# Kernel tuning notes

Measured on AMD Instinct MI355X. Metric: run time of the kernel, lower is better.

## Reference

```python
import jax, jax.numpy as jnp
import numpy as np

B, N, D, H = 4, 512, 3, 128


def _linear_params(key, fan_in, fan_out):
    kw, kb = jax.random.split(key)
    lim = 1.0 / np.sqrt(fan_in)
    W = jax.random.uniform(kw, (fan_in, fan_out), jnp.float32, -lim, lim)
    b = jax.random.uniform(kb, (fan_out,), jnp.float32, -lim, lim)
    return W, b


def setup_inputs() -> dict:
    key = jax.random.key(0)
    ks = jax.random.split(key, 9)
    x = jax.random.normal(ks[0], (B, N, D), jnp.float32)
    Ws1, bs1 = _linear_params(ks[1], D, H)   # make_features.single
    Wp1, bp1 = _linear_params(ks[2], D, H)   # make_features.pair
    Wc1s, bc1s = _linear_params(ks[3], H, H)  # combine1.single
    Wc1p, bc1p = _linear_params(ks[4], H, H)  # combine1.pair
    Wpl, bpl = _linear_params(ks[5], H, H)    # pair_lin
    Wc2s, bc2s = _linear_params(ks[6], H, D)  # combine2.single (random, not zero-init, to exercise full graph)
    Wc2p, bc2p = _linear_params(ks[7], H, D)  # combine2.pair
    Wskip = -jnp.eye(D, dtype=jnp.float32)    # skip.weight init = -I (applied as x @ Wskip.T)
    return dict(x=x, Ws1=Ws1, bs1=bs1, Wp1=Wp1, bp1=bp1,
                Wc1s=Wc1s, bc1s=bc1s, Wc1p=Wc1p, bc1p=bc1p,
                Wpl=Wpl, bpl=bpl, Wc2s=Wc2s, bc2s=bc2s,
                Wc2p=Wc2p, bc2p=bc2p, Wskip=Wskip)


def reference(x, Ws1, bs1, Wp1, bp1, Wc1s, bc1s, Wc1p, bc1p,
              Wpl, bpl, Wc2s, bc2s, Wc2p, bc2p, Wskip):
    ht = lambda v: jnp.clip(v, -1.0, 1.0)  # Hardtanh
    n = x.shape[-2]
    # pairs[..., i, j, :] = x[j] - x[i]
    pairs = x[..., None, :, :] - x[..., :, None, :]          # [B, N, N, D]
    s = ht(x @ Ws1 + bs1)                                    # [B, N, H]
    p = ht(pairs @ Wp1 + bp1)                                # [B, N, N, H]
    # combine1: single(s) + pair(p).sum(dim=-3); sum-then-matmul is identical math, cheaper
    s = s @ Wc1s + bc1s + (p.sum(axis=-3) @ Wc1p + n * bc1p)  # [B, N, H]
    p = p @ Wpl + bpl                                         # [B, N, N, H]
    s = ht(s)
    p = ht(p)
    out = s @ Wc2s + bc2s + (p.sum(axis=-3) @ Wc2p + n * bc2p)  # [B, N, D]
    out = out + x @ Wskip.T                                     # skip (bias-free linear)
    return out
```

## Files before the change

### kernel.cpp

```cpp
#include <hip/hip_runtime.h>
#include <hip/hip_bf16.h>


typedef float f32x4 __attribute__((ext_vector_type(4)));
typedef __bf16 bf16x8 __attribute__((ext_vector_type(8)));

union PKU { uint4 u; bf16x8 v; };

__device__ __forceinline__ float clamp1(float v) { return fminf(1.0f, fmaxf(-1.0f, v)); }
__device__ __forceinline__ unsigned f2bf(float f) {
    unsigned u = __float_as_uint(f);
    u += 0x7FFF + ((u >> 16) & 1);
    return u >> 16;
}

__global__ void prep_kernel(const float* __restrict__ x, const float* __restrict__ Wp1,
                            const float* __restrict__ Wpl,
                            float* __restrict__ q, unsigned* __restrict__ wsBf) {
    int gid = blockIdx.x * 256 + threadIdx.x;
    if (blockIdx.x < 1024) {
        int h = gid & 127, n = gid >> 7;
        const float* xp = x + n * 3;
        q[gid] = xp[0] * Wp1[h] + xp[1] * Wp1[128 + h] + xp[2] * Wp1[256 + h];
    } else {
        int g = gid - 1024 * 256;
        int w  = g & 3;
        int l  = (g >> 2) & 63;
        int fi = g >> 8;
        int wn = fi >> 4, nf = (fi >> 2) & 3, kf = fi & 3;
        int n = wn * 64 + nf * 16 + (l & 15);
        int k = kf * 32 + (l >> 4) * 8 + w * 2;
        unsigned lo = f2bf(Wpl[k * 128 + n]);
        unsigned hi = f2bf(Wpl[(k + 1) * 128 + n]);
        wsBf[g] = lo | (hi << 16);
    }
}

__global__ __launch_bounds__(256, 2) void pair_kernel(
    const float* __restrict__ q, const unsigned* __restrict__ wsBf,
    const float* __restrict__ bp1, const float* __restrict__ bpl,
    float* __restrict__ psum1, float* __restrict__ psum2)
{
    __shared__ uint4 A_lds[2048];
    __shared__ float ps1[16][128];
    __shared__ float ps2[2][128];

    const int tid  = threadIdx.x;
    const int lane = tid & 63;
    const int wid  = tid >> 6;
    const int wm = wid >> 1, wn = wid & 1;
    const int bj = blockIdx.x;
    const int b  = bj >> 9;
    const float* __restrict__ qb = q + (b << 9) * 128;

    bf16x8 Bf[4][4];
    #pragma unroll
    for (int nf = 0; nf < 4; ++nf)
        #pragma unroll
        for (int kf = 0; kf < 4; ++kf) {
            PKU t;
            t.u = *(const uint4*)(wsBf + ((((wn << 4) | (nf << 2) | kf) << 6) | lane) * 4);
            Bf[nf][kf] = t.v;
        }

    const int c = tid & 15, rb = tid >> 4;
    float qjb[8];
    {
        const float* qj = q + bj * 128 + c * 8;
        #pragma unroll
        for (int e = 0; e < 8; ++e) qjb[e] = qj[e] + bp1[c * 8 + e];
    }
    float bplv[4];
    #pragma unroll
    for (int nf = 0; nf < 4; ++nf) bplv[nf] = bpl[wn * 64 + nf * 16 + (lane & 15)];

    float psum1r[8] = {0, 0, 0, 0, 0, 0, 0, 0};
    f32x4 acc[4][4];
    #pragma unroll
    for (int mf = 0; mf < 4; ++mf)
        #pragma unroll
        for (int nf = 0; nf < 4; ++nf) acc[mf][nf] = (f32x4){0.f, 0.f, 0.f, 0.f};
    float colsum[4] = {0, 0, 0, 0};

    for (int ch = 0; ch < 4; ++ch) {
        #pragma unroll
        for (int u = 0; u < 8; ++u) {
            const int r = (u << 4) | rb;
            const int i = (ch << 7) | r;
            const float4 q0 = *(const float4*)(qb + i * 128 + c * 8);
            const float4 q1 = *(const float4*)(qb + i * 128 + c * 8 + 4);
            float p[8];
            p[0] = clamp1(qjb[0] - q0.x); p[1] = clamp1(qjb[1] - q0.y);
            p[2] = clamp1(qjb[2] - q0.z); p[3] = clamp1(qjb[3] - q0.w);
            p[4] = clamp1(qjb[4] - q1.x); p[5] = clamp1(qjb[5] - q1.y);
            p[6] = clamp1(qjb[6] - q1.z); p[7] = clamp1(qjb[7] - q1.w);
            #pragma unroll
            for (int e = 0; e < 8; ++e) psum1r[e] += p[e];
            uint4 pk;
            pk.x = f2bf(p[0]) | (f2bf(p[1]) << 16);
            pk.y = f2bf(p[2]) | (f2bf(p[3]) << 16);
            pk.z = f2bf(p[4]) | (f2bf(p[5]) << 16);
            pk.w = f2bf(p[6]) | (f2bf(p[7]) << 16);
            unsigned addr = (r << 8) | (c << 4);
            addr ^= ((r & 7) << 4);
            A_lds[addr >> 4] = pk;
        }
        __syncthreads();
        #pragma unroll
        for (int kf = 0; kf < 4; ++kf) {
            bf16x8 Af[4];
            #pragma unroll
            for (int mf = 0; mf < 4; ++mf) {
                const int row = wm * 64 + mf * 16 + (lane & 15);
                unsigned addr = (row << 8) + (kf << 6) + ((lane >> 4) << 4);
                addr ^= ((row & 7) << 4);
                PKU t; t.u = A_lds[addr >> 4];
                Af[mf] = t.v;
            }
            #pragma unroll
            for (int mf = 0; mf < 4; ++mf)
                #pragma unroll
                for (int nf = 0; nf < 4; ++nf)
                    acc[mf][nf] = __builtin_amdgcn_mfma_f32_16x16x32_bf16(
                        Af[mf], Bf[nf][kf], acc[mf][nf], 0, 0, 0);
        }
        __syncthreads();
        #pragma unroll
        for (int mf = 0; mf < 4; ++mf)
            #pragma unroll
            for (int nf = 0; nf < 4; ++nf) {
                f32x4 a = acc[mf][nf];
                acc[mf][nf] = (f32x4){0.f, 0.f, 0.f, 0.f};
                colsum[nf] += clamp1(a.x + bplv[nf]) + clamp1(a.y + bplv[nf])
                            + clamp1(a.z + bplv[nf]) + clamp1(a.w + bplv[nf]);
            }
    }

    *(float4*)(&ps1[rb][c * 8])     = make_float4(psum1r[0], psum1r[1], psum1r[2], psum1r[3]);
    *(float4*)(&ps1[rb][c * 8 + 4]) = make_float4(psum1r[4], psum1r[5], psum1r[6], psum1r[7]);
    #pragma unroll
    for (int nf = 0; nf < 4; ++nf) {
        float v = colsum[nf];
        v += __shfl_xor(v, 16);
        v += __shfl_xor(v, 32);
        if (lane < 16) ps2[wm][wn * 64 + nf * 16 + lane] = v;
    }
    __syncthreads();
    if (tid < 128) {
        float s = 0.f;
        #pragma unroll
        for (int r2 = 0; r2 < 16; ++r2) s += ps1[r2][tid];
        psum1[bj * 128 + tid] = s;
        psum2[bj * 128 + tid] = ps2[0][tid] + ps2[1][tid];
    }
}

__global__ void combine_kernel(
    const float* __restrict__ x,
    const float* __restrict__ Ws1, const float* __restrict__ bs1,
    const float* __restrict__ Wc1s, const float* __restrict__ bc1s,
    const float* __restrict__ Wc1p, const float* __restrict__ bc1p,
    const float* __restrict__ Wc2s, const float* __restrict__ bc2s,
    const float* __restrict__ Wc2p, const float* __restrict__ bc2p,
    const float* __restrict__ Wskip,
    const float* __restrict__ psum1, const float* __restrict__ psum2,
    float* __restrict__ out)
{
    __shared__ float s1[128], p1s[128], red[6];
    const int h = threadIdx.x;
    const int bj = blockIdx.x;
    const float* xj = x + bj * 3;

    float s1h = clamp1(xj[0] * Ws1[h] + xj[1] * Ws1[128 + h] + xj[2] * Ws1[256 + h] + bs1[h]);
    s1[h]  = s1h;
    p1s[h] = psum1[bj * 128 + h];
    __syncthreads();

    float s2 = bc1s[h] + 512.0f * bc1p[h];
    for (int k = 0; k < 128; ++k)
        s2 += s1[k] * Wc1s[k * 128 + h] + p1s[k] * Wc1p[k * 128 + h];
    float s3 = clamp1(s2);

    float ps2h = psum2[bj * 128 + h];
    float c0 = s3 * Wc2s[h * 3 + 0] + ps2h * Wc2p[h * 3 + 0];
    float c1 = s3 * Wc2s[h * 3 + 1] + ps2h * Wc2p[h * 3 + 1];
    float c2 = s3 * Wc2s[h * 3 + 2] + ps2h * Wc2p[h * 3 + 2];
    #pragma unroll
    for (int off = 32; off > 0; off >>= 1) {
        c0 += __shfl_down(c0, off);
        c1 += __shfl_down(c1, off);
        c2 += __shfl_down(c2, off);
    }
    if ((h & 63) == 0) {
        red[(h >> 6) * 3 + 0] = c0;
        red[(h >> 6) * 3 + 1] = c1;
        red[(h >> 6) * 3 + 2] = c2;
    }
    __syncthreads();
    if (h < 3) {
        float o = red[h] + red[3 + h];
        o += bc2s[h] + 512.0f * bc2p[h];
        o += xj[0] * Wskip[h * 3 + 0] + xj[1] * Wskip[h * 3 + 1] + xj[2] * Wskip[h * 3 + 2];
        out[bj * 3 + h] = o;
    }
}

extern "C" void kernel_launch(void* const* d_in, const int* in_sizes, int n_in,
                              void* d_out, int out_size, void* d_ws, size_t ws_size,
                              hipStream_t stream) {
    const float* x    = (const float*)d_in[0];
    const float* Ws1  = (const float*)d_in[1];
    const float* bs1  = (const float*)d_in[2];
    const float* Wp1  = (const float*)d_in[3];
    const float* bp1  = (const float*)d_in[4];
    const float* Wc1s = (const float*)d_in[5];
    const float* bc1s = (const float*)d_in[6];
    const float* Wc1p = (const float*)d_in[7];
    const float* bc1p = (const float*)d_in[8];
    const float* Wpl  = (const float*)d_in[9];
    const float* bpl  = (const float*)d_in[10];
    const float* Wc2s = (const float*)d_in[11];
    const float* bc2s = (const float*)d_in[12];
    const float* Wc2p = (const float*)d_in[13];
    const float* bc2p = (const float*)d_in[14];
    const float* Wskip= (const float*)d_in[15];

    float*    q    = (float*)d_ws;
    unsigned* wsBf = (unsigned*)((char*)d_ws + (1 << 20));
    float*    ps1  = (float*)((char*)d_ws + (1 << 20) + 32768);
    float*    ps2  = ps1 + 4 * 512 * 128;

    prep_kernel<<<1056, 256, 0, stream>>>(x, Wp1, Wpl, q, wsBf);
    pair_kernel<<<2048, 256, 0, stream>>>(q, wsBf, bp1, bpl, ps1, ps2);
    combine_kernel<<<2048, 128, 0, stream>>>(x, Ws1, bs1, Wc1s, bc1s, Wc1p, bc1p,
                                             Wc2s, bc2s, Wc2p, bc2p, Wskip,
                                             ps1, ps2, (float*)d_out);
}
```

Baseline: 167.0 us.

## Fuse combine stage into pair kernel and double-buffer the LDS A tile

```diff
diff --git a/kernel.cpp b/kernel.cpp
--- a/kernel.cpp
+++ b/kernel.cpp
@@ -7,22 +7,29 @@
 
 union PKU { uint4 u; bf16x8 v; };
 
-__device__ __forceinline__ float clamp1(float v) { return fminf(1.0f, fmaxf(-1.0f, v)); }
+__device__ __forceinline__ float ht1(float v) { return __builtin_amdgcn_fmed3f(v, -1.0f, 1.0f); }
 __device__ __forceinline__ unsigned f2bf(float f) {
     unsigned u = __float_as_uint(f);
     u += 0x7FFF + ((u >> 16) & 1);
     return u >> 16;
 }
+__device__ __forceinline__ unsigned cvtpk(float a, float b) {
+    unsigned r;
+    asm("v_cvt_pk_bf16_f32 %0, %1, %2" : "=v"(r) : "v"(a), "v"(b));
+    return r;
+}
 
 __global__ void prep_kernel(const float* __restrict__ x, const float* __restrict__ Wp1,
                             const float* __restrict__ Wpl,
-                            float* __restrict__ q, unsigned* __restrict__ wsBf) {
+                            const float* __restrict__ Wc1s, const float* __restrict__ Wc1p,
+                            float* __restrict__ q, unsigned* __restrict__ wsBf,
+                            float* __restrict__ wt1s, float* __restrict__ wt1p) {
     int gid = blockIdx.x * 256 + threadIdx.x;
     if (blockIdx.x < 1024) {
         int h = gid & 127, n = gid >> 7;
         const float* xp = x + n * 3;
         q[gid] = xp[0] * Wp1[h] + xp[1] * Wp1[128 + h] + xp[2] * Wp1[256 + h];
-    } else {
+    } else if (blockIdx.x < 1056) {
         int g = gid - 1024 * 256;
         int w  = g & 3;
         int l  = (g >> 2) & 63;
@@ -33,17 +40,32 @@
         unsigned lo = f2bf(Wpl[k * 128 + n]);
         unsigned hi = f2bf(Wpl[(k + 1) * 128 + n]);
         wsBf[g] = lo | (hi << 16);
+    } else {
+        int g = gid - 1056 * 256;
+        int m = g >> 14;
+        int e = g & 16383;
+        int h = e >> 7, k = e & 127;
+        if (m) wt1p[e] = Wc1p[k * 128 + h];
+        else   wt1s[e] = Wc1s[k * 128 + h];
     }
 }
 
 __global__ __launch_bounds__(256, 2) void pair_kernel(
     const float* __restrict__ q, const unsigned* __restrict__ wsBf,
     const float* __restrict__ bp1, const float* __restrict__ bpl,
-    float* __restrict__ psum1, float* __restrict__ psum2)
+    const float* __restrict__ x,
+    const float* __restrict__ Ws1, const float* __restrict__ bs1,
+    const float* __restrict__ wt1s, const float* __restrict__ wt1p,
+    const float* __restrict__ bc1s, const float* __restrict__ bc1p,
+    const float* __restrict__ Wc2s, const float* __restrict__ bc2s,
+    const float* __restrict__ Wc2p, const float* __restrict__ bc2p,
+    const float* __restrict__ Wskip,
+    float* __restrict__ out)
 {
-    __shared__ uint4 A_lds[2048];
+    __shared__ uint4 A_lds[2][2048];
     __shared__ float ps1[16][128];
     __shared__ float ps2[2][128];
+    __shared__ float s1l[128], p1l[128], s2p[2][128], red[8];
 
     const int tid  = threadIdx.x;
     const int lane = tid & 63;
@@ -76,13 +98,11 @@
 
     float psum1r[8] = {0, 0, 0, 0, 0, 0, 0, 0};
     f32x4 acc[4][4];
-    #pragma unroll
-    for (int mf = 0; mf < 4; ++mf)
-        #pragma unroll
-        for (int nf = 0; nf < 4; ++nf) acc[mf][nf] = (f32x4){0.f, 0.f, 0.f, 0.f};
     float colsum[4] = {0, 0, 0, 0};
+    const f32x4 zf = (f32x4){0.f, 0.f, 0.f, 0.f};
 
     for (int ch = 0; ch < 4; ++ch) {
+        uint4* __restrict__ Ab = A_lds[ch & 1];
         #pragma unroll
         for (int u = 0; u < 8; ++u) {
             const int r = (u << 4) | rb;
@@ -90,20 +110,20 @@
             const float4 q0 = *(const float4*)(qb + i * 128 + c * 8);
             const float4 q1 = *(const float4*)(qb + i * 128 + c * 8 + 4);
             float p[8];
-            p[0] = clamp1(qjb[0] - q0.x); p[1] = clamp1(qjb[1] - q0.y);
-            p[2] = clamp1(qjb[2] - q0.z); p[3] = clamp1(qjb[3] - q0.w);
-            p[4] = clamp1(qjb[4] - q1.x); p[5] = clamp1(qjb[5] - q1.y);
-            p[6] = clamp1(qjb[6] - q1.z); p[7] = clamp1(qjb[7] - q1.w);
+            p[0] = ht1(qjb[0] - q0.x); p[1] = ht1(qjb[1] - q0.y);
+            p[2] = ht1(qjb[2] - q0.z); p[3] = ht1(qjb[3] - q0.w);
+            p[4] = ht1(qjb[4] - q1.x); p[5] = ht1(qjb[5] - q1.y);
+            p[6] = ht1(qjb[6] - q1.z); p[7] = ht1(qjb[7] - q1.w);
             #pragma unroll
             for (int e = 0; e < 8; ++e) psum1r[e] += p[e];
             uint4 pk;
-            pk.x = f2bf(p[0]) | (f2bf(p[1]) << 16);
-            pk.y = f2bf(p[2]) | (f2bf(p[3]) << 16);
-            pk.z = f2bf(p[4]) | (f2bf(p[5]) << 16);
-            pk.w = f2bf(p[6]) | (f2bf(p[7]) << 16);
+            pk.x = cvtpk(p[0], p[1]);
+            pk.y = cvtpk(p[2], p[3]);
+            pk.z = cvtpk(p[4], p[5]);
+            pk.w = cvtpk(p[6], p[7]);
             unsigned addr = (r << 8) | (c << 4);
             addr ^= ((r & 7) << 4);
-            A_lds[addr >> 4] = pk;
+            Ab[addr >> 4] = pk;
         }
         __syncthreads();
         #pragma unroll
@@ -114,7 +134,7 @@
                 const int row = wm * 64 + mf * 16 + (lane & 15);
                 unsigned addr = (row << 8) + (kf << 6) + ((lane >> 4) << 4);
                 addr ^= ((row & 7) << 4);
-                PKU t; t.u = A_lds[addr >> 4];
+                PKU t; t.u = Ab[addr >> 4];
                 Af[mf] = t.v;
             }
             #pragma unroll
@@ -122,17 +142,15 @@
                 #pragma unroll
                 for (int nf = 0; nf < 4; ++nf)
                     acc[mf][nf] = __builtin_amdgcn_mfma_f32_16x16x32_bf16(
-                        Af[mf], Bf[nf][kf], acc[mf][nf], 0, 0, 0);
-        }
-        __syncthreads();
+                        Af[mf], Bf[nf][kf], kf == 0 ? zf : acc[mf][nf], 0, 0, 0);
+        }
         #pragma unroll
         for (int mf = 0; mf < 4; ++mf)
             #pragma unroll
             for (int nf = 0; nf < 4; ++nf) {
                 f32x4 a = acc[mf][nf];
-                acc[mf][nf] = (f32x4){0.f, 0.f, 0.f, 0.f};
-                colsum[nf] += clamp1(a.x + bplv[nf]) + clamp1(a.y + bplv[nf])
-                            + clamp1(a.z + bplv[nf]) + clamp1(a.w + bplv[nf]);
+                colsum[nf] += ht1(a.x + bplv[nf]) + ht1(a.y + bplv[nf])
+                            + ht1(a.z + bplv[nf]) + ht1(a.w + bplv[nf]);
             }
     }
 
@@ -146,62 +164,60 @@
         if (lane < 16) ps2[wm][wn * 64 + nf * 16 + lane] = v;
     }
     __syncthreads();
+
+    const int h = tid & 127;
     if (tid < 128) {
         float s = 0.f;
         #pragma unroll
         for (int r2 = 0; r2 < 16; ++r2) s += ps1[r2][tid];
-        psum1[bj * 128 + tid] = s;
-        psum2[bj * 128 + tid] = ps2[0][tid] + ps2[1][tid];
-    }
-}
-
-__global__ void combine_kernel(
-    const float* __restrict__ x,
-    const float* __restrict__ Ws1, const float* __restrict__ bs1,
-    const float* __restrict__ Wc1s, const float* __restrict__ bc1s,
-    const float* __restrict__ Wc1p, const float* __restrict__ bc1p,
-    const float* __restrict__ Wc2s, const float* __restrict__ bc2s,
-    const float* __restrict__ Wc2p, const float* __restrict__ bc2p,
-    const float* __restrict__ Wskip,
-    const float* __restrict__ psum1, const float* __restrict__ psum2,
-    float* __restrict__ out)
-{
-    __shared__ float s1[128], p1s[128], red[6];
-    const int h = threadIdx.x;
-    const int bj = blockIdx.x;
-    const float* xj = x + bj * 3;
-
-    float s1h = clamp1(xj[0] * Ws1[h] + xj[1] * Ws1[128 + h] + xj[2] * Ws1[256 + h] + bs1[h]);
-    s1[h]  = s1h;
-    p1s[h] = psum1[bj * 128 + h];
-    __syncthreads();
-
-    float s2 = bc1s[h] + 512.0f * bc1p[h];
-    for (int k = 0; k < 128; ++k)
-        s2 += s1[k] * Wc1s[k * 128 + h] + p1s[k] * Wc1p[k * 128 + h];
-    float s3 = clamp1(s2);
-
-    float ps2h = psum2[bj * 128 + h];
-    float c0 = s3 * Wc2s[h * 3 + 0] + ps2h * Wc2p[h * 3 + 0];
-    float c1 = s3 * Wc2s[h * 3 + 1] + ps2h * Wc2p[h * 3 + 1];
-    float c2 = s3 * Wc2s[h * 3 + 2] + ps2h * Wc2p[h * 3 + 2];
-    #pragma unroll
-    for (int off = 32; off > 0; off >>= 1) {
-        c0 += __shfl_down(c0, off);
-        c1 += __shfl_down(c1, off);
-        c2 += __shfl_down(c2, off);
-    }
-    if ((h & 63) == 0) {
-        red[(h >> 6) * 3 + 0] = c0;
-        red[(h >> 6) * 3 + 1] = c1;
-        red[(h >> 6) * 3 + 2] = c2;
-    }
-    __syncthreads();
-    if (h < 3) {
-        float o = red[h] + red[3 + h];
-        o += bc2s[h] + 512.0f * bc2p[h];
-        o += xj[0] * Wskip[h * 3 + 0] + xj[1] * Wskip[h * 3 + 1] + xj[2] * Wskip[h * 3 + 2];
-        out[bj * 3 + h] = o;
+        p1l[tid] = s;
+        const float* xj = x + bj * 3;
+        s1l[tid] = ht1(xj[0] * Ws1[tid] + xj[1] * Ws1[128 + tid] + xj[2] * Ws1[256 + tid] + bs1[tid]);
+    }
+    __syncthreads();
+
+    {
+        const int half = tid >> 7;
+        const float* w1 = wt1s + h * 128 + half * 64;
+        const float* w2 = wt1p + h * 128 + half * 64;
+        float a2 = 0.f;
+        #pragma unroll
+        for (int k = 0; k < 64; k += 4) {
+            float4 wa = *(const float4*)(w1 + k);
+            float4 wb = *(const float4*)(w2 + k);
+            const int kk = half * 64 + k;
+            a2 += wa.x * s1l[kk] + wa.y * s1l[kk + 1] + wa.z * s1l[kk + 2] + wa.w * s1l[kk + 3];
+            a2 += wb.x * p1l[kk] + wb.y * p1l[kk + 1] + wb.z * p1l[kk + 2] + wb.w * p1l[kk + 3];
+        }
+        s2p[half][h] = a2;
+    }
+    __syncthreads();
+
+    if (tid < 128) {
+        float s3 = ht1(s2p[0][tid] + s2p[1][tid] + bc1s[tid] + 512.0f * bc1p[tid]);
+        float pp = ps2[0][tid] + ps2[1][tid];
+        float c0 = s3 * Wc2s[tid * 3 + 0] + pp * Wc2p[tid * 3 + 0];
+        float c1 = s3 * Wc2s[tid * 3 + 1] + pp * Wc2p[tid * 3 + 1];
+        float c2 = s3 * Wc2s[tid * 3 + 2] + pp * Wc2p[tid * 3 + 2];
+        #pragma unroll
+        for (int off = 32; off > 0; off >>= 1) {
+            c0 += __shfl_down(c0, off);
+            c1 += __shfl_down(c1, off);
+            c2 += __shfl_down(c2, off);
+        }
+        if (lane == 0) {
+            red[wid * 3 + 0] = c0;
+            red[wid * 3 + 1] = c1;
+            red[wid * 3 + 2] = c2;
+        }
+    }
+    __syncthreads();
+    if (tid < 3) {
+        const float* xj = x + bj * 3;
+        float o = red[tid] + red[3 + tid];
+        o += bc2s[tid] + 512.0f * bc2p[tid];
+        o += xj[0] * Wskip[tid * 3 + 0] + xj[1] * Wskip[tid * 3 + 1] + xj[2] * Wskip[tid * 3 + 2];
+        out[bj * 3 + tid] = o;
     }
 }
 
@@ -227,12 +243,12 @@
 
     float*    q    = (float*)d_ws;
     unsigned* wsBf = (unsigned*)((char*)d_ws + (1 << 20));
-    float*    ps1  = (float*)((char*)d_ws + (1 << 20) + 32768);
-    float*    ps2  = ps1 + 4 * 512 * 128;
-
-    prep_kernel<<<1056, 256, 0, stream>>>(x, Wp1, Wpl, q, wsBf);
-    pair_kernel<<<2048, 256, 0, stream>>>(q, wsBf, bp1, bpl, ps1, ps2);
-    combine_kernel<<<2048, 128, 0, stream>>>(x, Ws1, bs1, Wc1s, bc1s, Wc1p, bc1p,
-                                             Wc2s, bc2s, Wc2p, bc2p, Wskip,
-                                             ps1, ps2, (float*)d_out);
-}
+    float*    wt1s = (float*)((char*)d_ws + (1 << 20) + 32768);
+    float*    wt1p = wt1s + 16384;
+
+    prep_kernel<<<1184, 256, 0, stream>>>(x, Wp1, Wpl, Wc1s, Wc1p, q, wsBf, wt1s, wt1p);
+    pair_kernel<<<2048, 256, 0, stream>>>(q, wsBf, bp1, bpl, x, Ws1, bs1,
+                                          wt1s, wt1p, bc1s, bc1p,
+                                          Wc2s, bc2s, Wc2p, bc2p, Wskip,
+                                          (float*)d_out);
+}
```

Measured after the change: 179.0 us. +7.1%, slower.
